# Kernel tuning notes

Measured on AMD Instinct MI355X. Metric: run time of the kernel, lower is better.

The kernel has to match this reference:

```python
import jax, jax.numpy as jnp
import numpy as np

N, D, C, P = 4096, 512, 100, 64
EPS_COS = 1e-8   # torch cosine_similarity norm clamp
EPS_INV = 1e-5   # module's 1/(d + 1e-5)


def setup_inputs() -> dict:
    key = jax.random.key(0)
    k1, k2, k3, k4 = jax.random.split(key, 4)
    feats = jax.random.normal(k1, (N, D), dtype=jnp.float32)
    protos = jax.random.normal(k2, (C, P, D), dtype=jnp.float32)
    cls_ids = jax.random.randint(k3, (N,), 0, C)
    proto_labels = jax.random.randint(k4, (C, P), 0, 1000)
    return {"feats": feats, "protos": protos, "cls_ids": cls_ids,
            "proto_labels": proto_labels}


def reference(feats, protos, cls_ids, proto_labels):
    # Gather each box's class-conditional prototype set: [N, P, D]
    p = protos[cls_ids]
    pl = proto_labels[cls_ids]                       # [N, P]

    # cosine distance: 1 - f.p / (max(|f|,eps) * max(|p|,eps))
    dot = jnp.einsum('nd,npd->np', feats, p)         # [N, P]
    fnorm = jnp.maximum(jnp.linalg.norm(feats, axis=-1, keepdims=True), EPS_COS)
    pnorm = jnp.maximum(jnp.linalg.norm(p, axis=-1), EPS_COS)
    d_cos = 1.0 - dot / (fnorm * pnorm)

    diff = feats[:, None, :] - p                     # [N, P, D]
    d_l1 = jnp.mean(jnp.abs(diff), axis=-1)          # F.l1_loss (mean)
    d_l2 = jnp.mean(diff * diff, axis=-1)            # F.mse_loss (mean)

    dists = jnp.stack([d_cos, d_l1, d_l2], axis=1)   # [N, 3, P]
    probs = jax.nn.softmax(1.0 / (dists + EPS_INV), axis=-1).mean(axis=1)  # [N, P]

    idx = jnp.argmax(probs, axis=-1)                 # [N]
    labels = jnp.take_along_axis(pl, idx[:, None], axis=1)[:, 0]
    return labels, probs
```

## Files before the change

### kernel.cpp

```cpp
#include <hip/hip_runtime.h>

#define D 512
#define P 64
#define CHUNK 16
#define MAXDESC 384
#define EPS_COS 1e-8f
#define EPS_INV 1e-5f


__device__ __forceinline__ float wave_sum(float v) {
#pragma unroll
    for (int m = 32; m >= 1; m >>= 1) v += __shfl_xor(v, m, 64);
    return v;
}

__global__ __launch_bounds__(256) void proto_norm_kernel(
    const float* __restrict__ protos, float* __restrict__ pp, int rows)
{
    const int lane = threadIdx.x & 63;
    const int r = blockIdx.x * 4 + (threadIdx.x >> 6);
    if (r >= rows) return;
    const float* row = protos + (size_t)r * D;
    const float4 a = *(const float4*)(row + lane * 4);
    const float4 b = *(const float4*)(row + 256 + lane * 4);
    float s = a.x*a.x + a.y*a.y + a.z*a.z + a.w*a.w
            + b.x*b.x + b.y*b.y + b.z*b.z + b.w*b.w;
    s = wave_sum(s);
    if (lane == 0) pp[r] = s;
}

__global__ __launch_bounds__(1024) void setup_kernel(
    const int* __restrict__ cls, int* __restrict__ sorted,
    int* __restrict__ desc, int* __restrict__ ndesc, int N, int C)
{
    __shared__ int cnt[128], fl[128], exc[128], gexc[128];
    const int t = threadIdx.x;
    if (t < 128) { cnt[t] = 0; fl[t] = 0; }
    __syncthreads();
#pragma unroll
    for (int k = 0; k < 4; ++k) {
        const int n = t + 1024 * k;
        if (n < N) atomicAdd(&cnt[cls[n]], 1);
    }
    __syncthreads();
    int v = 0, gv = 0;
    if (t < 128) { v = cnt[t]; gv = (v + CHUNK - 1) / CHUNK; exc[t] = v; gexc[t] = gv; }
    __syncthreads();
    for (int d = 1; d < 128; d <<= 1) {
        int a = 0, b = 0;
        if (t < 128 && t >= d) { a = exc[t - d]; b = gexc[t - d]; }
        __syncthreads();
        if (t < 128 && t >= d) { exc[t] += a; gexc[t] += b; }
        __syncthreads();
    }
    int base = 0, gbase = 0;
    if (t < 128) { base = exc[t] - v; gbase = gexc[t] - gv; }
    if (t == 127) ndesc[0] = gexc[127];
    if (t < 128) exc[t] = base;
    __syncthreads();
    if (t < C) {
        for (int k = 0; k < gv; ++k) {
            desc[3*(gbase+k)+0] = t;
            desc[3*(gbase+k)+1] = base + CHUNK*k;
            desc[3*(gbase+k)+2] = min(CHUNK, v - CHUNK*k);
        }
    }
#pragma unroll
    for (int k = 0; k < 4; ++k) {
        const int n = t + 1024 * k;
        if (n < N) {
            const int c = cls[n];
            const int pos = exc[c] + atomicAdd(&fl[c], 1);
            sorted[pos] = n;
        }
    }
}

__global__ __launch_bounds__(512, 2) void proto_main_kernel(
    const float* __restrict__ feats,
    const float* __restrict__ protos,
    const int*   __restrict__ proto_labels,
    const float* __restrict__ ppbuf,
    const int*   __restrict__ sorted,
    const int*   __restrict__ desc,
    const int*   __restrict__ ndesc,
    float* __restrict__ out, int N)
{
    __shared__ float tile[16 * D];
    __shared__ float dist[CHUNK * P * 2];
    __shared__ float ffbuf[CHUNK];

    if ((int)blockIdx.x >= ndesc[0]) return;
    const int cls   = desc[3*blockIdx.x];
    const int start = desc[3*blockIdx.x+1];
    const int cnt   = desc[3*blockIdx.x+2];
    const int tid  = threadIdx.x;
    const int lane = tid & 63;
    const int wave = tid >> 6;
    const int bg = wave & 3;
    const int h  = wave >> 2;

    int nidx[4];
#pragma unroll
    for (int k = 0; k < 4; ++k) {
        const int pos = bg + 4*k;
        nidx[k] = sorted[start + (pos < cnt ? pos : cnt - 1)];
    }

    float4 f0[4], f1[4];
    float  ff[4];
#pragma unroll
    for (int b = 0; b < 4; ++b) {
        const float* f = feats + (size_t)nidx[b] * D;
        f0[b] = *(const float4*)(f + lane * 4);
        f1[b] = *(const float4*)(f + 256 + lane * 4);
        float s = f0[b].x*f0[b].x + f0[b].y*f0[b].y + f0[b].z*f0[b].z + f0[b].w*f0[b].w
                + f1[b].x*f1[b].x + f1[b].y*f1[b].y + f1[b].z*f1[b].z + f1[b].w*f1[b].w;
        ff[b] = wave_sum(s);
    }
    if (h == 0 && lane == 0) {
#pragma unroll
        for (int k = 0; k < 4; ++k) ffbuf[bg + 4*k] = ff[k];
    }

    const float* pr = protos + (size_t)cls * (P * D);
    const bool hi32 = (lane & 32) != 0;
    const bool hi16 = (lane & 16) != 0;
    const bool hi8  = (lane & 8)  != 0;

    float r_dot[4] = {0.f,0.f,0.f,0.f}, r_l1[4] = {0.f,0.f,0.f,0.f};

    for (int pass = 0; pass < 4; ++pass) {
        if (pass) __syncthreads();
#pragma unroll
        for (int i = 0; i < 4; ++i) {
            const int idx = tid + 512 * i;
            *(float4*)(tile + idx * 4) =
                *(const float4*)(pr + pass * (16 * D) + idx * 4);
        }
        __syncthreads();

        float pd[4][8], pl[4][8];
#pragma unroll
        for (int j = 0; j < 8; ++j) {
            const float* row = tile + (8 * h + j) * D;
            const float4 q0 = *(const float4*)(row + lane * 4);
            const float4 q1 = *(const float4*)(row + 256 + lane * 4);
#pragma unroll
            for (int b = 0; b < 4; ++b) {
                float dot, l1, t;
                dot  = f0[b].x*q0.x; t = f0[b].x - q0.x; l1  = fabsf(t);
                dot += f0[b].y*q0.y; t = f0[b].y - q0.y; l1 += fabsf(t);
                dot += f0[b].z*q0.z; t = f0[b].z - q0.z; l1 += fabsf(t);
                dot += f0[b].w*q0.w; t = f0[b].w - q0.w; l1 += fabsf(t);
                dot += f1[b].x*q1.x; t = f1[b].x - q1.x; l1 += fabsf(t);
                dot += f1[b].y*q1.y; t = f1[b].y - q1.y; l1 += fabsf(t);
                dot += f1[b].z*q1.z; t = f1[b].z - q1.z; l1 += fabsf(t);
                dot += f1[b].w*q1.w; t = f1[b].w - q1.w; l1 += fabsf(t);
                pd[b][j] = dot; pl[b][j] = l1;
            }
        }
#pragma unroll
        for (int b = 0; b < 4; ++b) {
#pragma unroll
            for (int k = 0; k < 4; ++k) {
                const float sd = hi32 ? pd[b][k] : pd[b][k+4];
                const float sl = hi32 ? pl[b][k] : pl[b][k+4];
                const float rd = __shfl_xor(sd, 32, 64);
                const float rl = __shfl_xor(sl, 32, 64);
                pd[b][k] = (hi32 ? pd[b][k+4] : pd[b][k]) + rd;
                pl[b][k] = (hi32 ? pl[b][k+4] : pl[b][k]) + rl;
            }
#pragma unroll
            for (int k = 0; k < 2; ++k) {
                const float sd = hi16 ? pd[b][k] : pd[b][k+2];
                const float sl = hi16 ? pl[b][k] : pl[b][k+2];
                const float rd = __shfl_xor(sd, 16, 64);
                const float rl = __shfl_xor(sl, 16, 64);
                pd[b][k] = (hi16 ? pd[b][k+2] : pd[b][k]) + rd;
                pl[b][k] = (hi16 ? pl[b][k+2] : pl[b][k]) + rl;
            }
            {
                const float sd = hi8 ? pd[b][0] : pd[b][1];
                const float sl = hi8 ? pl[b][0] : pl[b][1];
                const float rd = __shfl_xor(sd, 8, 64);
                const float rl = __shfl_xor(sl, 8, 64);
                pd[b][0] = (hi8 ? pd[b][1] : pd[b][0]) + rd;
                pl[b][0] = (hi8 ? pl[b][1] : pl[b][0]) + rl;
            }
#pragma unroll
            for (int m = 4; m >= 1; m >>= 1) {
                pd[b][0] += __shfl_xor(pd[b][0], m, 64);
                pl[b][0] += __shfl_xor(pl[b][0], m, 64);
            }
            if ((lane & 3) == pass) { r_dot[b] = pd[b][0]; r_l1[b] = pl[b][0]; }
        }
    }

    {
        const int pg   = 16 * (lane & 3) + 8 * h + ((lane >> 3) & 7);
        const int qsel = (lane >> 2) & 1;
#pragma unroll
        for (int k = 0; k < 4; ++k) {
            dist[((bg + 4*k) * P + pg) * 2 + qsel] = qsel ? r_l1[k] : r_dot[k];
        }
    }
    __syncthreads();

    const float ppv   = ppbuf[cls * P + lane];
    const float pnorm = fmaxf(sqrtf(ppv), EPS_COS);

#pragma unroll
    for (int kk = 0; kk < 2; ++kk) {
        const int s = 2 * wave + kk;
        if (s >= cnt) continue;
        const int n = sorted[start + s];
        const float2 dl = *(const float2*)&dist[(s * P + lane) * 2];
        const float ffv   = ffbuf[s];
        const float fnorm = fmaxf(sqrtf(ffv), EPS_COS);
        const float d_cos = 1.0f - dl.x / (fnorm * pnorm);
        const float d_l1  = dl.y * (1.0f / (float)D);
        const float d_l2  = (ffv - 2.0f * dl.x + ppv) * (1.0f / (float)D);

        float sc[3];
        sc[0] = 1.0f / (d_cos + EPS_INV);
        sc[1] = 1.0f / (d_l1  + EPS_INV);
        sc[2] = 1.0f / (d_l2  + EPS_INV);

        float prob = 0.f;
#pragma unroll
        for (int i = 0; i < 3; ++i) {
            float m = sc[i];
#pragma unroll
            for (int w = 32; w >= 1; w >>= 1) m = fmaxf(m, __shfl_xor(m, w, 64));
            const float e = expf(sc[i] - m);
            prob += e / wave_sum(e);
        }
        prob *= (1.0f / 3.0f);

        float best = prob;
        int   bidx = lane;
#pragma unroll
        for (int w = 32; w >= 1; w >>= 1) {
            const float ov = __shfl_xor(best, w, 64);
            const int   oi = __shfl_xor(bidx, w, 64);
            if (ov > best || (ov == best && oi < bidx)) { best = ov; bidx = oi; }
        }

        out[(size_t)N + (size_t)n * P + lane] = prob;
        if (lane == 0) out[n] = (float)proto_labels[cls * P + bidx];
    }
}

extern "C" void kernel_launch(void* const* d_in, const int* in_sizes, int n_in,
                              void* d_out, int out_size, void* d_ws, size_t ws_size,
                              hipStream_t stream) {
    const float* feats        = (const float*)d_in[0];
    const float* protos       = (const float*)d_in[1];
    const int*   cls_ids      = (const int*)d_in[2];
    const int*   proto_labels = (const int*)d_in[3];
    float* out = (float*)d_out;

    const int N    = in_sizes[2];
    const int rows = in_sizes[1] / D;
    const int C    = rows / P;

    char* w = (char*)d_ws;
    float* pp     = (float*)w;
    int*   sorted = (int*)(w + 25600);
    int*   desc   = (int*)(w + 41984);
    int*   ndesc  = (int*)(w + 46592);

    proto_norm_kernel<<<(rows + 3) / 4, 256, 0, stream>>>(protos, pp, rows);
    setup_kernel<<<1, 1024, 0, stream>>>(cls_ids, sorted, desc, ndesc, N, C);
    proto_main_kernel<<<MAXDESC, 512, 0, stream>>>(
        feats, protos, proto_labels, pp, sorted, desc, ndesc, out, N);
}
```

Baseline: 123.3 us.

## Split main kernel into distance and softmax kernels with half-prototype blocks

Replaces the single fused kernel with two kernels. A distance kernel runs per chunk-half, with 256 threads and 32 prototypes per block, reads prototypes straight from global memory with no LDS tile or barriers, and writes dot/L1 partials to a workspace buffer. A separate softmax kernel then computes the feature norms and the softmax/argmax per row. Chunk descriptors are interleaved into four buckets across a fixed grid of 2*1152 blocks, with empty slots exiting early. The aim is more blocks, better occupancy and no LDS sync stalls, at the cost of an extra launch, a global round trip for distances, and repeated prototype loads from global/L2.

```diff
diff --git a/kernel.cpp b/kernel.cpp
--- a/kernel.cpp
+++ b/kernel.cpp
@@ -3,7 +3,7 @@
 #define D 512
 #define P 64
 #define CHUNK 16
-#define MAXDESC 384
+#define MAXD 1152
 #define EPS_COS 1e-8f
 #define EPS_INV 1e-5f
 
@@ -31,11 +31,12 @@
 
 __global__ __launch_bounds__(1024) void setup_kernel(
     const int* __restrict__ cls, int* __restrict__ sorted,
-    int* __restrict__ desc, int* __restrict__ ndesc, int N, int C)
-{
-    __shared__ int cnt[128], fl[128], exc[128], gexc[128];
+    int* __restrict__ desc, int N, int C)
+{
+    __shared__ int cnt[128], fl[128], exc[128], arr[128];
     const int t = threadIdx.x;
-    if (t < 128) { cnt[t] = 0; fl[t] = 0; }
+    if (t < 128) { cnt[t] = 0; fl[t] = 0; arr[t] = 0; }
+    for (int i = t; i < 3 * MAXD; i += 1024) desc[i] = 0;
     __syncthreads();
 #pragma unroll
     for (int k = 0; k < 4; ++k) {
@@ -43,26 +44,36 @@
         if (n < N) atomicAdd(&cnt[cls[n]], 1);
     }
     __syncthreads();
-    int v = 0, gv = 0;
-    if (t < 128) { v = cnt[t]; gv = (v + CHUNK - 1) / CHUNK; exc[t] = v; gexc[t] = gv; }
+    int v = 0, gv = 0, pos = 0;
+    if (t < 128) {
+        v = cnt[t];
+        gv = (v + CHUNK - 1) / CHUNK;
+        pos = ((t & 3) << 5) | (t >> 2);
+        exc[t] = v;
+        arr[pos] = gv;
+    }
     __syncthreads();
     for (int d = 1; d < 128; d <<= 1) {
         int a = 0, b = 0;
-        if (t < 128 && t >= d) { a = exc[t - d]; b = gexc[t - d]; }
+        if (t < 128 && t >= d) { a = exc[t - d]; b = arr[t - d]; }
         __syncthreads();
-        if (t < 128 && t >= d) { exc[t] += a; gexc[t] += b; }
+        if (t < 128 && t >= d) { exc[t] += a; arr[t] += b; }
         __syncthreads();
     }
-    int base = 0, gbase = 0;
-    if (t < 128) { base = exc[t] - v; gbase = gexc[t] - gv; }
-    if (t == 127) ndesc[0] = gexc[127];
+    int base = 0;
+    if (t < 128) base = exc[t] - v;
+    __syncthreads();
     if (t < 128) exc[t] = base;
     __syncthreads();
-    if (t < C) {
+    if (t < C && gv > 0) {
+        const int b = t & 3;
+        const int bstart = (pos >= 32) ? arr[(pos & ~31) - 1] : 0;
+        const int localoff = (arr[pos] - gv) - bstart;
         for (int k = 0; k < gv; ++k) {
-            desc[3*(gbase+k)+0] = t;
-            desc[3*(gbase+k)+1] = base + CHUNK*k;
-            desc[3*(gbase+k)+2] = min(CHUNK, v - CHUNK*k);
+            const int slot = ((localoff + k) << 2) | b;
+            desc[3*slot+0] = t;
+            desc[3*slot+1] = base + CHUNK * k;
+            desc[3*slot+2] = min(CHUNK, v - CHUNK * k);
         }
     }
 #pragma unroll
@@ -70,80 +81,57 @@
         const int n = t + 1024 * k;
         if (n < N) {
             const int c = cls[n];
-            const int pos = exc[c] + atomicAdd(&fl[c], 1);
-            sorted[pos] = n;
-        }
-    }
-}
-
-__global__ __launch_bounds__(512, 2) void proto_main_kernel(
+            const int p2 = exc[c] + atomicAdd(&fl[c], 1);
+            sorted[p2] = n;
+        }
+    }
+}
+
+__global__ __launch_bounds__(256, 3) void proto_dist_kernel(
     const float* __restrict__ feats,
     const float* __restrict__ protos,
-    const int*   __restrict__ proto_labels,
-    const float* __restrict__ ppbuf,
     const int*   __restrict__ sorted,
     const int*   __restrict__ desc,
-    const int*   __restrict__ ndesc,
-    float* __restrict__ out, int N)
-{
-    __shared__ float tile[16 * D];
-    __shared__ float dist[CHUNK * P * 2];
-    __shared__ float ffbuf[CHUNK];
-
-    if ((int)blockIdx.x >= ndesc[0]) return;
-    const int cls   = desc[3*blockIdx.x];
-    const int start = desc[3*blockIdx.x+1];
-    const int cnt   = desc[3*blockIdx.x+2];
-    const int tid  = threadIdx.x;
-    const int lane = tid & 63;
-    const int wave = tid >> 6;
-    const int bg = wave & 3;
-    const int h  = wave >> 2;
-
-    int nidx[4];
-#pragma unroll
-    for (int k = 0; k < 4; ++k) {
-        const int pos = bg + 4*k;
-        nidx[k] = sorted[start + (pos < cnt ? pos : cnt - 1)];
+    float* __restrict__ dist)
+{
+    const int di   = blockIdx.x >> 1;
+    const int half = blockIdx.x & 1;
+    const int cnt  = desc[3*di+2];
+    if (cnt == 0) return;
+    const int cls   = desc[3*di+0];
+    const int start = desc[3*di+1];
+    const int lane = threadIdx.x & 63;
+    const int wave = threadIdx.x >> 6;
+
+    int  nidx[4];
+    bool valid[4];
+#pragma unroll
+    for (int k = 0; k < 4; ++k) {
+        const int pos = wave + 4 * k;
+        valid[k] = pos < cnt;
+        nidx[k]  = sorted[start + (valid[k] ? pos : (cnt - 1))];
     }
 
     float4 f0[4], f1[4];
-    float  ff[4];
 #pragma unroll
     for (int b = 0; b < 4; ++b) {
         const float* f = feats + (size_t)nidx[b] * D;
         f0[b] = *(const float4*)(f + lane * 4);
         f1[b] = *(const float4*)(f + 256 + lane * 4);
-        float s = f0[b].x*f0[b].x + f0[b].y*f0[b].y + f0[b].z*f0[b].z + f0[b].w*f0[b].w
-                + f1[b].x*f1[b].x + f1[b].y*f1[b].y + f1[b].z*f1[b].z + f1[b].w*f1[b].w;
-        ff[b] = wave_sum(s);
-    }
-    if (h == 0 && lane == 0) {
-#pragma unroll
-        for (int k = 0; k < 4; ++k) ffbuf[bg + 4*k] = ff[k];
-    }
-
-    const float* pr = protos + (size_t)cls * (P * D);
+    }
+
+    const float* pr = protos + (size_t)cls * (P * D) + (size_t)half * (32 * D);
     const bool hi32 = (lane & 32) != 0;
     const bool hi16 = (lane & 16) != 0;
     const bool hi8  = (lane & 8)  != 0;
 
-    float r_dot[4] = {0.f,0.f,0.f,0.f}, r_l1[4] = {0.f,0.f,0.f,0.f};
-
-    for (int pass = 0; pass < 4; ++pass) {
-        if (pass) __syncthreads();
-#pragma unroll
-        for (int i = 0; i < 4; ++i) {
-            const int idx = tid + 512 * i;
-            *(float4*)(tile + idx * 4) =
-                *(const float4*)(pr + pass * (16 * D) + idx * 4);
-        }
-        __syncthreads();
-
+    float r_dot[4], r_l1[4];
+
+    for (int g = 0; g < 4; ++g) {
         float pd[4][8], pl[4][8];
 #pragma unroll
         for (int j = 0; j < 8; ++j) {
-            const float* row = tile + (8 * h + j) * D;
+            const float* row = pr + (size_t)(8 * g + j) * D;
             const float4 q0 = *(const float4*)(row + lane * 4);
             const float4 q1 = *(const float4*)(row + 256 + lane * 4);
 #pragma unroll
@@ -193,63 +181,75 @@
                 pd[b][0] += __shfl_xor(pd[b][0], m, 64);
                 pl[b][0] += __shfl_xor(pl[b][0], m, 64);
             }
-            if ((lane & 3) == pass) { r_dot[b] = pd[b][0]; r_l1[b] = pl[b][0]; }
-        }
-    }
-
-    {
-        const int pg   = 16 * (lane & 3) + 8 * h + ((lane >> 3) & 7);
-        const int qsel = (lane >> 2) & 1;
-#pragma unroll
-        for (int k = 0; k < 4; ++k) {
-            dist[((bg + 4*k) * P + pg) * 2 + qsel] = qsel ? r_l1[k] : r_dot[k];
-        }
-    }
-    __syncthreads();
-
+            if ((lane & 3) == g) { r_dot[b] = pd[b][0]; r_l1[b] = pl[b][0]; }
+        }
+    }
+
+    const int pg   = 32 * half + 8 * (lane & 3) + ((lane >> 3) & 7);
+    const int qsel = (lane >> 2) & 1;
+#pragma unroll
+    for (int k = 0; k < 4; ++k) {
+        if (valid[k]) {
+            dist[((size_t)nidx[k] * P + pg) * 2 + qsel] = qsel ? r_l1[k] : r_dot[k];
+        }
+    }
+}
+
+__global__ __launch_bounds__(256) void softmax_kernel(
+    const float* __restrict__ feats,
+    const int*   __restrict__ cls_ids,
+    const int*   __restrict__ proto_labels,
+    const float* __restrict__ ppbuf,
+    const float* __restrict__ dist,
+    float* __restrict__ out, int N)
+{
+    const int lane = threadIdx.x & 63;
+    const int n = blockIdx.x * 4 + (threadIdx.x >> 6);
+    if (n >= N) return;
+    const int cls = cls_ids[n];
+
+    const float* f = feats + (size_t)n * D;
+    const float4 a = *(const float4*)(f + lane * 4);
+    const float4 b = *(const float4*)(f + 256 + lane * 4);
+    float ffv = a.x*a.x + a.y*a.y + a.z*a.z + a.w*a.w
+              + b.x*b.x + b.y*b.y + b.z*b.z + b.w*b.w;
+    ffv = wave_sum(ffv);
+
+    const float2 dl = *(const float2*)&dist[((size_t)n * P + lane) * 2];
     const float ppv   = ppbuf[cls * P + lane];
+    const float fnorm = fmaxf(sqrtf(ffv), EPS_COS);
     const float pnorm = fmaxf(sqrtf(ppv), EPS_COS);
-
-#pragma unroll
-    for (int kk = 0; kk < 2; ++kk) {
-        const int s = 2 * wave + kk;
-        if (s >= cnt) continue;
-        const int n = sorted[start + s];
-        const float2 dl = *(const float2*)&dist[(s * P + lane) * 2];
-        const float ffv   = ffbuf[s];
-        const float fnorm = fmaxf(sqrtf(ffv), EPS_COS);
-        const float d_cos = 1.0f - dl.x / (fnorm * pnorm);
-        const float d_l1  = dl.y * (1.0f / (float)D);
-        const float d_l2  = (ffv - 2.0f * dl.x + ppv) * (1.0f / (float)D);
-
-        float sc[3];
-        sc[0] = 1.0f / (d_cos + EPS_INV);
-        sc[1] = 1.0f / (d_l1  + EPS_INV);
-        sc[2] = 1.0f / (d_l2  + EPS_INV);
-
-        float prob = 0.f;
-#pragma unroll
-        for (int i = 0; i < 3; ++i) {
-            float m = sc[i];
-#pragma unroll
-            for (int w = 32; w >= 1; w >>= 1) m = fmaxf(m, __shfl_xor(m, w, 64));
-            const float e = expf(sc[i] - m);
-            prob += e / wave_sum(e);
-        }
-        prob *= (1.0f / 3.0f);
-
-        float best = prob;
-        int   bidx = lane;
-#pragma unroll
-        for (int w = 32; w >= 1; w >>= 1) {
-            const float ov = __shfl_xor(best, w, 64);
-            const int   oi = __shfl_xor(bidx, w, 64);
-            if (ov > best || (ov == best && oi < bidx)) { best = ov; bidx = oi; }
-        }
-
-        out[(size_t)N + (size_t)n * P + lane] = prob;
-        if (lane == 0) out[n] = (float)proto_labels[cls * P + bidx];
-    }
+    const float d_cos = 1.0f - dl.x / (fnorm * pnorm);
+    const float d_l1  = dl.y * (1.0f / (float)D);
+    const float d_l2  = (ffv - 2.0f * dl.x + ppv) * (1.0f / (float)D);
+
+    float sc[3];
+    sc[0] = 1.0f / (d_cos + EPS_INV);
+    sc[1] = 1.0f / (d_l1  + EPS_INV);
+    sc[2] = 1.0f / (d_l2  + EPS_INV);
+
+    float prob = 0.f;
+#pragma unroll
+    for (int i = 0; i < 3; ++i) {
+        float m = sc[i];
+#pragma unroll
+        for (int w = 32; w >= 1; w >>= 1) m = fmaxf(m, __shfl_xor(m, w, 64));
+        const float e = expf(sc[i] - m);
+        prob += e / wave_sum(e);
+    }
+    prob *= (1.0f / 3.0f);
+
+    float best = prob;
+    int   bidx = lane;
+#pragma unroll
+    for (int w = 32; w >= 1; w >>= 1) {
+        const float ov = __shfl_xor(best, w, 64);
+        const int   oi = __shfl_xor(bidx, w, 64);
+        if (ov > best || (ov == best && oi < bidx)) { best = ov; bidx = oi; }
+    }
+
+    out[(size_t)N + (size_t)n * P + lane] = prob;
+    if (lane == 0) out[n] = (float)proto_labels[cls * P + bidx];
 }
 
 extern "C" void kernel_launch(void* const* d_in, const int* in_sizes, int n_in,
@@ -269,10 +269,11 @@
     float* pp     = (float*)w;
     int*   sorted = (int*)(w + 25600);
     int*   desc   = (int*)(w + 41984);
-    int*   ndesc  = (int*)(w + 46592);
+    float* dist   = (float*)(w + 57344);
 
     proto_norm_kernel<<<(rows + 3) / 4, 256, 0, stream>>>(protos, pp, rows);
-    setup_kernel<<<1, 1024, 0, stream>>>(cls_ids, sorted, desc, ndesc, N, C);
-    proto_main_kernel<<<MAXDESC, 512, 0, stream>>>(
-        feats, protos, proto_labels, pp, sorted, desc, ndesc, out, N);
-}
+    setup_kernel<<<1, 1024, 0, stream>>>(cls_ids, sorted, desc, N, C);
+    proto_dist_kernel<<<2 * MAXD, 256, 0, stream>>>(feats, protos, sorted, desc, dist);
+    softmax_kernel<<<(N + 3) / 4, 256, 0, stream>>>(
+        feats, cls_ids, proto_labels, pp, dist, out, N);
+}
```

After: 119.8 us. 1.03x faster.
